# Kernel optimization log

Measured on AMD Instinct MI355X. Metric: run time of the kernel, lower is better.

Reference implementation:

```python
import jax, jax.numpy as jnp
import numpy as np

D_MODEL = 1024
NUM_HEADS = 16
HEAD_DIM = D_MODEL // NUM_HEADS
SCALE = HEAD_DIM ** -0.5
ROPE_BASE = 10000.0


def _rope_cos_sin(seq_len, dim, dtype=jnp.float32):
    inv_freq = 1.0 / (ROPE_BASE ** (jnp.arange(0, dim, 2, dtype=jnp.float32) / dim))
    t = jnp.arange(seq_len, dtype=jnp.float32)
    freqs = t[:, None] * inv_freq[None, :]            # [S, dim/2]
    emb = jnp.concatenate([freqs, freqs], axis=-1)    # [S, dim]
    # broadcast shape [1, S, 1, dim] to apply over [B, S, H, dim]
    return emb.astype(dtype)[None, :, None, :]


def _rotate_half(x):
    half = x.shape[-1] // 2
    x1, x2 = x[..., :half], x[..., half:]
    return jnp.concatenate([-x2, x1], axis=-1)


def setup_inputs() -> dict:
    key = jax.random.key(0)
    ks = jax.random.split(key, 5)
    B, S = 2, 2048
    x = jax.random.normal(ks[0], (B, S, D_MODEL), dtype=jnp.float32)
    wq = jax.random.normal(ks[1], (D_MODEL, D_MODEL), dtype=jnp.float32) * (D_MODEL ** -0.5)
    wk = jax.random.normal(ks[2], (D_MODEL, D_MODEL), dtype=jnp.float32) * (D_MODEL ** -0.5)
    wv = jax.random.normal(ks[3], (D_MODEL, D_MODEL), dtype=jnp.float32) * (D_MODEL ** -0.5)
    wo = jax.random.normal(ks[4], (D_MODEL, D_MODEL), dtype=jnp.float32) * (D_MODEL ** -0.5)
    attention_mask = jnp.tril(jnp.ones((S, S), dtype=jnp.int32))  # causal
    return {"x": x, "wq": wq, "wk": wk, "wv": wv, "wo": wo,
            "attention_mask": attention_mask}


def reference(x, wq, wk, wv, wo, attention_mask):
    B, S, _ = x.shape
    # projections (nn.Linear, no bias: y = x @ W^T)
    q = (x @ wq.T).reshape(B, S, NUM_HEADS, HEAD_DIM)
    k = (x @ wk.T).reshape(B, S, NUM_HEADS, HEAD_DIM)
    v = (x @ wv.T).reshape(B, S, NUM_HEADS, HEAD_DIM)
    # RoPE
    emb = _rope_cos_sin(S, HEAD_DIM, x.dtype)
    cos, sin = jnp.cos(emb), jnp.sin(emb)
    q = q * cos + _rotate_half(q) * sin
    k = k * cos + _rotate_half(k) * sin
    # attention scores [B, H, S, S]
    scores = jnp.einsum('bihd,bjhd->bhij', q, k) * SCALE
    mask = attention_mask[None, None, :, :]  # 2D mask -> broadcast over batch, heads
    scores = jnp.where(mask == 0, -jnp.inf, scores)
    attn = jax.nn.softmax(scores, axis=-1)
    attn = jnp.nan_to_num(attn, nan=0.0)  # fully-masked rows -> 0
    out = jnp.einsum('bhij,bjhd->bihd', attn, v).reshape(B, S, D_MODEL)
    return out @ wo.T
```

## Files before the change

kernel.cpp:

```cpp
#include <hip/hip_runtime.h>

typedef __bf16 bf16;
typedef __attribute__((ext_vector_type(8))) __bf16 bf16x8;
typedef __attribute__((ext_vector_type(4))) float f32x4;
typedef __attribute__((ext_vector_type(4))) short s16x4;
typedef __attribute__((ext_vector_type(4))) unsigned u32x4;

#define SEQ 2048
#define DM 1024
#define NH 16
#define HD 64
#define QSCALE 0.1803368801111204f

static __device__ __forceinline__ void gl_lds16(const bf16* g, bf16* l) {
  __builtin_amdgcn_global_load_lds(
      (const __attribute__((address_space(1))) void*)g,
      (__attribute__((address_space(3))) void*)l, 16, 0, 0);
}

static __device__ __forceinline__ f32x4 mfma16(bf16x8 a, bf16x8 b, f32x4 c) {
  return __builtin_amdgcn_mfma_f32_16x16x32_bf16(a, b, c, 0, 0, 0);
}

static __device__ __forceinline__ unsigned cvt_pk_bf16(float lo, float hi) {
  unsigned r;
  asm("v_cvt_pk_bf16_f32 %0, %1, %2" : "=v"(r) : "v"(lo), "v"(hi));
  return r;
}

static __device__ __forceinline__ float vmax4(f32x4 v) {
  return fmaxf(fmaxf(v[0], v[1]), fmaxf(v[2], v[3]));
}

__global__ __launch_bounds__(256)
void prep_k(const float* __restrict__ x, const float* __restrict__ wq,
            const float* __restrict__ wk, const float* __restrict__ wv,
            const float* __restrict__ wo, bf16* __restrict__ xb,
            bf16* __restrict__ wb, float* __restrict__ tab) {
  int i = blockIdx.x * 256 + threadIdx.x;
  if (i < 2097152) {
    const float* src;
    bf16* dst;
    int j;
    if (i < 1048576) {
      src = x; dst = xb; j = i;
    } else {
      j = i - 1048576;
      int seg = j >> 18;
      src = (seg == 0) ? wq : (seg == 1) ? wk : (seg == 2) ? wv : wo;
      dst = wb;
      src -= (size_t)seg << 20;
    }
    f32x4 v = ((const f32x4*)src)[j];
    s16x4 o;
#pragma unroll
    for (int q = 0; q < 4; ++q) o[q] = __builtin_bit_cast(short, (bf16)v[q]);
    ((s16x4*)dst)[j] = o;
  } else {
    int idx = i - 2097152;
    int s = idx >> 5, j = idx & 31;
    float inv = powf(10000.0f, -(float)j * (1.0f / 32.0f));
    float f = (float)s * inv;
    tab[idx * 2] = cosf(f);
    tab[idx * 2 + 1] = sinf(f);
  }
}

__global__ __launch_bounds__(256)
void gemm_qkv(const bf16* __restrict__ A, const bf16* __restrict__ B,
              bf16* __restrict__ qh, bf16* __restrict__ kh, bf16* __restrict__ vt,
              const float2* __restrict__ tab) {
  const int K = 1024;
  __shared__ __attribute__((aligned(16))) bf16 As[128 * 32];
  __shared__ __attribute__((aligned(16))) bf16 Bs[128 * 32];
  const int t = threadIdx.x;
  const int wv = t >> 6, ln = t & 63, lr = ln & 15, lg = ln >> 4;
  const int wr = wv >> 1, wc = wv & 1;
  const int l_hw = blockIdx.x + 24 * blockIdx.y;
  const int lid = (l_hw & 7) * 96 + (l_hw >> 3);
  const int m0 = (lid / 24) * 128, n0 = (lid % 24) * 128;
  const int srow = t >> 2, sslot = t & 3;
  const int seg = n0 >> 10;
  const int hh = ((n0 & 1023) + wc * 64) >> 6;

  f32x4 acc[4][4] = {};

  for (int kt = 0; kt < K; kt += 32) {
#pragma unroll
    for (int c = 0; c < 2; ++c) {
      int row = srow + (c << 6);
      int lsl = sslot ^ (row & 3);
      gl_lds16(A + (size_t)(m0 + row) * K + kt + lsl * 8, As + c * 2048 + wv * 512);
      gl_lds16(B + (size_t)(n0 + row) * K + kt + lsl * 8, Bs + c * 2048 + wv * 512);
    }
    __syncthreads();
    bf16x8 af[4], bfr[4];
#pragma unroll
    for (int i = 0; i < 4; ++i) {
      int ra = wr * 64 + i * 16 + lr;
      af[i] = *(const bf16x8*)(As + ra * 32 + ((lg ^ (ra & 3)) << 3));
      int rb = wc * 64 + i * 16 + lr;
      bfr[i] = *(const bf16x8*)(Bs + rb * 32 + ((lg ^ (rb & 3)) << 3));
    }
#pragma unroll
    for (int i = 0; i < 4; ++i)
#pragma unroll
      for (int j = 0; j < 4; ++j)
        acc[i][j] = mfma16(af[i], bfr[j], acc[i][j]);
    __syncthreads();
  }

#pragma unroll
  for (int i = 0; i < 4; ++i) {
    int row0 = m0 + wr * 64 + i * 16 + lg * 4;
    int bb = row0 >> 11, s0r = row0 & (SEQ - 1);
    if (seg < 2) {
      bf16* dst = (seg == 0) ? qh : kh;
      float scl = (seg == 0) ? QSCALE : 1.0f;
      size_t base = ((size_t)(bb * NH + hh) * SEQ + s0r) * HD;
#pragma unroll
      for (int j = 0; j < 2; ++j) {
        int dlo = j * 16 + lr;
#pragma unroll
        for (int r = 0; r < 4; ++r) {
          float2 cs = tab[(size_t)(s0r + r) * 32 + dlo];
          float a = acc[i][j][r], b2 = acc[i][j + 2][r];
          float na = (a * cs.x - b2 * cs.y) * scl;
          float nb = (b2 * cs.x + a * cs.y) * scl;
          dst[base + (size_t)r * HD + dlo] = (bf16)na;
          dst[base + (size_t)r * HD + dlo + 32] = (bf16)nb;
        }
      }
    } else {
#pragma unroll
      for (int j = 0; j < 4; ++j) {
        int d = j * 16 + lr;
        s16x4 pk;
#pragma unroll
        for (int r = 0; r < 4; ++r) pk[r] = __builtin_bit_cast(short, (bf16)acc[i][j][r]);
        *(s16x4*)(vt + ((size_t)(bb * NH + hh) * HD + d) * SEQ + s0r) = pk;
      }
    }
  }
}

__global__ __launch_bounds__(256)
void gemm_bt_f32(const bf16* __restrict__ A, const bf16* __restrict__ B,
                 float* __restrict__ C, int M, int N, int K) {
  __shared__ __attribute__((aligned(16))) bf16 As[128 * 32];
  __shared__ __attribute__((aligned(16))) bf16 Bs[128 * 32];
  const int t = threadIdx.x;
  const int wv = t >> 6, ln = t & 63, lr = ln & 15, lg = ln >> 4;
  const int wr = wv >> 1, wc = wv & 1;
  const int l_hw = blockIdx.x + 8 * blockIdx.y;
  const int lid = (l_hw & 7) * 32 + (l_hw >> 3);
  const int m0 = (lid >> 3) * 128, n0 = (lid & 7) * 128;
  const int srow = t >> 2, sslot = t & 3;

  f32x4 acc[4][4] = {};

  for (int kt = 0; kt < K; kt += 32) {
#pragma unroll
    for (int c = 0; c < 2; ++c) {
      int row = srow + (c << 6);
      int lsl = sslot ^ (row & 3);
      gl_lds16(A + (size_t)(m0 + row) * K + kt + lsl * 8, As + c * 2048 + wv * 512);
      gl_lds16(B + (size_t)(n0 + row) * K + kt + lsl * 8, Bs + c * 2048 + wv * 512);
    }
    __syncthreads();
    bf16x8 af[4], bfr[4];
#pragma unroll
    for (int i = 0; i < 4; ++i) {
      int ra = wr * 64 + i * 16 + lr;
      af[i] = *(const bf16x8*)(As + ra * 32 + ((lg ^ (ra & 3)) << 3));
      int rb = wc * 64 + i * 16 + lr;
      bfr[i] = *(const bf16x8*)(Bs + rb * 32 + ((lg ^ (rb & 3)) << 3));
    }
#pragma unroll
    for (int i = 0; i < 4; ++i)
#pragma unroll
      for (int j = 0; j < 4; ++j)
        acc[i][j] = mfma16(af[i], bfr[j], acc[i][j]);
    __syncthreads();
  }

#pragma unroll
  for (int i = 0; i < 4; ++i) {
    int row0 = m0 + wr * 64 + i * 16 + lg * 4;
#pragma unroll
    for (int j = 0; j < 4; ++j) {
      int col = n0 + wc * 64 + j * 16 + lr;
#pragma unroll
      for (int r = 0; r < 4; ++r)
        C[(size_t)(row0 + r) * N + col] = acc[i][j][r];
    }
  }
}

template <bool MASKED>
static __device__ __forceinline__ void attn_tile_lds(
    const bf16* Ksb, const bf16* Vsb, unsigned* plw,
    const bf16x8* qf, f32x4* acc, float& m_run, float& l_run,
    int lr, int lg, int qrow, int s0) {
  f32x4 sc[4] = {};
#pragma unroll
  for (int fi = 0; fi < 4; ++fi) {
    int row = fi * 16 + lr;
    int sw = row & 7;
    bf16x8 k0 = *(const bf16x8*)(Ksb + row * 64 + ((lg ^ sw) << 3));
    bf16x8 k1 = *(const bf16x8*)(Ksb + row * 64 + (((4 + lg) ^ sw) << 3));
    sc[fi] = mfma16(k0, qf[0], sc[fi]);
    sc[fi] = mfma16(k1, qf[1], sc[fi]);
  }
  if (MASKED) {
#pragma unroll
    for (int fi = 0; fi < 4; ++fi)
#pragma unroll
      for (int r = 0; r < 4; ++r) {
        int kv = s0 + fi * 16 + lg * 4 + r;
        sc[fi][r] = (kv <= qrow) ? sc[fi][r] : -3e38f;
      }
  }
  float mx = fmaxf(fmaxf(vmax4(sc[0]), vmax4(sc[1])),
                   fmaxf(vmax4(sc[2]), vmax4(sc[3])));
  mx = fmaxf(mx, __shfl_xor(mx, 16));
  mx = fmaxf(mx, __shfl_xor(mx, 32));
  if (!__all(mx <= m_run)) {
    float mn = fmaxf(m_run, mx);
    float alpha = __builtin_amdgcn_exp2f(m_run - mn);
    m_run = mn;
    l_run *= alpha;
#pragma unroll
    for (int d0 = 0; d0 < 4; ++d0)
#pragma unroll
      for (int r = 0; r < 4; ++r) acc[d0][r] *= alpha;
  }
  float pf[4][4], sm = 0.0f;
#pragma unroll
  for (int fi = 0; fi < 4; ++fi)
#pragma unroll
    for (int r = 0; r < 4; ++r) {
      pf[fi][r] = __builtin_amdgcn_exp2f(sc[fi][r] - m_run);
      sm += pf[fi][r];
    }
  sm += __shfl_xor(sm, 16);
  sm += __shfl_xor(sm, 32);
  l_run += sm;

  const int sw2 = (lr & 7) << 2;
#pragma unroll
  for (int fi = 0; fi < 4; ++fi)
#pragma unroll
    for (int hh = 0; hh < 2; ++hh)
      plw[lr * 32 + ((fi * 8 + lg * 2 + hh) ^ sw2)] =
          cvt_pk_bf16(pf[fi][2 * hh], pf[fi][2 * hh + 1]);
  asm volatile("s_waitcnt lgkmcnt(0)" ::: "memory");
  __builtin_amdgcn_sched_barrier(0);
#pragma unroll
  for (int kc = 0; kc < 2; ++kc) {
    u32x4 praw = *(const u32x4*)(plw + lr * 32 + ((kc * 16 + lg * 4) ^ sw2));
    bf16x8 pb = __builtin_bit_cast(bf16x8, praw);
#pragma unroll
    for (int d0 = 0; d0 < 4; ++d0) {
      int row = d0 * 16 + lr;
      int sw = row & 7;
      bf16x8 vf = *(const bf16x8*)(Vsb + row * 64 + (((kc * 4 + lg) ^ sw) << 3));
      acc[d0] = mfma16(vf, pb, acc[d0]);
    }
  }
  asm volatile("" ::: "memory");
}

__global__ __launch_bounds__(256, 4)
void attn_k(const bf16* __restrict__ qh, const bf16* __restrict__ kh,
            const bf16* __restrict__ vt, bf16* __restrict__ ao) {
  __shared__ __attribute__((aligned(16))) bf16 Ks[2][64 * 64];
  __shared__ __attribute__((aligned(16))) bf16 Vs[2][64 * 64];
  __shared__ __attribute__((aligned(16))) unsigned plds[4][512];

  const int t = threadIdx.x, wv = t >> 6, ln = t & 63, lr = ln & 15, lg = ln >> 4;
  const int bid = blockIdx.x;
  const int xcd = bid & 7, g = bid >> 3;
  const int bh = xcd * 4 + (g & 3);
  const int qt = 31 - (g >> 2);
  const int b = bh >> 4, h = bh & 15;

  const bf16* qp = qh + (size_t)bh * SEQ * HD;
  const bf16* kp = kh + (size_t)bh * SEQ * HD;
  const bf16* vp = vt + (size_t)bh * HD * SEQ;
  unsigned* plw = &plds[wv][0];

  const int qrow = qt * 64 + wv * 16 + lr;

  bf16x8 qf[2];
  qf[0] = *(const bf16x8*)(qp + (size_t)qrow * HD + lg * 8);
  qf[1] = *(const bf16x8*)(qp + (size_t)qrow * HD + 32 + lg * 8);

  f32x4 acc[4] = {};
  float m_run = -3e38f, l_run = 0.0f;

  const int nt = qt + 1;

  auto STAGE = [&](int buf, int tt) {
    int s0 = tt * 64;
#pragma unroll
    for (int c = 0; c < 2; ++c) {
      int rA = wv * 16 + c * 8;
      int row = rA + (ln >> 3);
      int sl = (ln & 7) ^ (row & 7);
      gl_lds16(kp + (size_t)(s0 + row) * HD + (sl << 3), &Ks[buf][rA * 64]);
      gl_lds16(vp + (size_t)row * SEQ + s0 + (sl << 3), &Vs[buf][rA * 64]);
    }
  };

  STAGE(0, 0);
  asm volatile("s_waitcnt vmcnt(0)" ::: "memory");
  __builtin_amdgcn_s_barrier();

  int cur = 0;
  for (int tt = 0; tt < nt; ++tt) {
    if (tt + 1 < nt) STAGE(cur ^ 1, tt + 1);
    if (tt == qt)
      attn_tile_lds<true>(&Ks[cur][0], &Vs[cur][0], plw, qf, acc, m_run, l_run,
                          lr, lg, qrow, tt * 64);
    else
      attn_tile_lds<false>(&Ks[cur][0], &Vs[cur][0], plw, qf, acc, m_run, l_run,
                           lr, lg, qrow, tt * 64);
    asm volatile("s_waitcnt vmcnt(0)" ::: "memory");
    __builtin_amdgcn_s_barrier();
    cur ^= 1;
  }

  float invl = 1.0f / l_run;
  bf16* aop = ao + ((size_t)b * SEQ + qrow) * DM + h * HD;
#pragma unroll
  for (int d0 = 0; d0 < 4; ++d0) {
    unsigned lo = cvt_pk_bf16(acc[d0][0] * invl, acc[d0][1] * invl);
    unsigned hi = cvt_pk_bf16(acc[d0][2] * invl, acc[d0][3] * invl);
    uint2 pk; pk.x = lo; pk.y = hi;
    *(uint2*)(aop + d0 * 16 + lg * 4) = pk;
  }
}

extern "C" void kernel_launch(void* const* d_in, const int* in_sizes, int n_in,
                              void* d_out, int out_size, void* d_ws, size_t ws_size,
                              hipStream_t stream) {
  const float* x = (const float*)d_in[0];
  const float* wq = (const float*)d_in[1];
  const float* wk = (const float*)d_in[2];
  const float* wv = (const float*)d_in[3];
  const float* wo = (const float*)d_in[4];

  char* ws = (char*)d_ws;
  const size_t MB = 1ull << 20;
  bf16* xb    = (bf16*)ws;
  bf16* wqkvb = (bf16*)(ws + 8 * MB);
  bf16* wob   = (bf16*)(ws + 14 * MB);
  bf16* qhb   = (bf16*)(ws + 16 * MB);
  bf16* khb   = (bf16*)(ws + 24 * MB);
  bf16* vtb   = (bf16*)(ws + 32 * MB);
  float* tab  = (float*)(ws + 40 * MB);
  bf16* aob = xb;

  prep_k<<<8448, 256, 0, stream>>>(x, wq, wk, wv, wo, xb, wqkvb, tab);

  gemm_qkv<<<dim3(24, 32), 256, 0, stream>>>(xb, wqkvb, qhb, khb, vtb, (const float2*)tab);

  attn_k<<<1024, 256, 0, stream>>>(qhb, khb, vtb, aob);

  gemm_bt_f32<<<dim3(8, 32), 256, 0, stream>>>(aob, wob, (float*)d_out, 4096, 1024, 1024);
}
```

Measured before the change: 118.8 us.

## Double-buffer LDS tiles in QKV and output projection GEMMs

Both projection GEMMs now use two LDS buffers per operand and issue the global-to-LDS loads for the next K-tile before computing on the current one. A single vmcnt wait and barrier per iteration replaces the two syncthreads. This is meant to overlap global memory latency with MFMA work. It doubles LDS use per block, which may lower occupancy.

```diff
diff --git a/kernel.cpp b/kernel.cpp
--- a/kernel.cpp
+++ b/kernel.cpp
@@ -71,8 +71,8 @@
               bf16* __restrict__ qh, bf16* __restrict__ kh, bf16* __restrict__ vt,
               const float2* __restrict__ tab) {
   const int K = 1024;
-  __shared__ __attribute__((aligned(16))) bf16 As[128 * 32];
-  __shared__ __attribute__((aligned(16))) bf16 Bs[128 * 32];
+  __shared__ __attribute__((aligned(16))) bf16 As[2][128 * 32];
+  __shared__ __attribute__((aligned(16))) bf16 Bs[2][128 * 32];
   const int t = threadIdx.x;
   const int wv = t >> 6, ln = t & 63, lr = ln & 15, lg = ln >> 4;
   const int wr = wv >> 1, wc = wv & 1;
@@ -85,29 +85,39 @@
 
   f32x4 acc[4][4] = {};
 
-  for (int kt = 0; kt < K; kt += 32) {
+  auto STAGE = [&](int buf, int kt) {
 #pragma unroll
     for (int c = 0; c < 2; ++c) {
       int row = srow + (c << 6);
       int lsl = sslot ^ (row & 3);
-      gl_lds16(A + (size_t)(m0 + row) * K + kt + lsl * 8, As + c * 2048 + wv * 512);
-      gl_lds16(B + (size_t)(n0 + row) * K + kt + lsl * 8, Bs + c * 2048 + wv * 512);
-    }
-    __syncthreads();
+      gl_lds16(A + (size_t)(m0 + row) * K + kt + lsl * 8, &As[buf][0] + c * 2048 + wv * 512);
+      gl_lds16(B + (size_t)(n0 + row) * K + kt + lsl * 8, &Bs[buf][0] + c * 2048 + wv * 512);
+    }
+  };
+
+  STAGE(0, 0);
+  asm volatile("s_waitcnt vmcnt(0)" ::: "memory");
+  __builtin_amdgcn_s_barrier();
+
+  int cur = 0;
+  for (int kt = 0; kt < K; kt += 32) {
+    if (kt + 32 < K) STAGE(cur ^ 1, kt + 32);
     bf16x8 af[4], bfr[4];
 #pragma unroll
     for (int i = 0; i < 4; ++i) {
       int ra = wr * 64 + i * 16 + lr;
-      af[i] = *(const bf16x8*)(As + ra * 32 + ((lg ^ (ra & 3)) << 3));
+      af[i] = *(const bf16x8*)(&As[cur][0] + ra * 32 + ((lg ^ (ra & 3)) << 3));
       int rb = wc * 64 + i * 16 + lr;
-      bfr[i] = *(const bf16x8*)(Bs + rb * 32 + ((lg ^ (rb & 3)) << 3));
+      bfr[i] = *(const bf16x8*)(&Bs[cur][0] + rb * 32 + ((lg ^ (rb & 3)) << 3));
     }
 #pragma unroll
     for (int i = 0; i < 4; ++i)
 #pragma unroll
       for (int j = 0; j < 4; ++j)
         acc[i][j] = mfma16(af[i], bfr[j], acc[i][j]);
-    __syncthreads();
+    asm volatile("s_waitcnt vmcnt(0)" ::: "memory");
+    __builtin_amdgcn_s_barrier();
+    cur ^= 1;
   }
 
 #pragma unroll
@@ -147,8 +157,8 @@
 __global__ __launch_bounds__(256)
 void gemm_bt_f32(const bf16* __restrict__ A, const bf16* __restrict__ B,
                  float* __restrict__ C, int M, int N, int K) {
-  __shared__ __attribute__((aligned(16))) bf16 As[128 * 32];
-  __shared__ __attribute__((aligned(16))) bf16 Bs[128 * 32];
+  __shared__ __attribute__((aligned(16))) bf16 As[2][128 * 32];
+  __shared__ __attribute__((aligned(16))) bf16 Bs[2][128 * 32];
   const int t = threadIdx.x;
   const int wv = t >> 6, ln = t & 63, lr = ln & 15, lg = ln >> 4;
   const int wr = wv >> 1, wc = wv & 1;
@@ -159,29 +169,39 @@
 
   f32x4 acc[4][4] = {};
 
-  for (int kt = 0; kt < K; kt += 32) {
+  auto STAGE = [&](int buf, int kt) {
 #pragma unroll
     for (int c = 0; c < 2; ++c) {
       int row = srow + (c << 6);
       int lsl = sslot ^ (row & 3);
-      gl_lds16(A + (size_t)(m0 + row) * K + kt + lsl * 8, As + c * 2048 + wv * 512);
-      gl_lds16(B + (size_t)(n0 + row) * K + kt + lsl * 8, Bs + c * 2048 + wv * 512);
-    }
-    __syncthreads();
+      gl_lds16(A + (size_t)(m0 + row) * K + kt + lsl * 8, &As[buf][0] + c * 2048 + wv * 512);
+      gl_lds16(B + (size_t)(n0 + row) * K + kt + lsl * 8, &Bs[buf][0] + c * 2048 + wv * 512);
+    }
+  };
+
+  STAGE(0, 0);
+  asm volatile("s_waitcnt vmcnt(0)" ::: "memory");
+  __builtin_amdgcn_s_barrier();
+
+  int cur = 0;
+  for (int kt = 0; kt < K; kt += 32) {
+    if (kt + 32 < K) STAGE(cur ^ 1, kt + 32);
     bf16x8 af[4], bfr[4];
 #pragma unroll
     for (int i = 0; i < 4; ++i) {
       int ra = wr * 64 + i * 16 + lr;
-      af[i] = *(const bf16x8*)(As + ra * 32 + ((lg ^ (ra & 3)) << 3));
+      af[i] = *(const bf16x8*)(&As[cur][0] + ra * 32 + ((lg ^ (ra & 3)) << 3));
       int rb = wc * 64 + i * 16 + lr;
-      bfr[i] = *(const bf16x8*)(Bs + rb * 32 + ((lg ^ (rb & 3)) << 3));
+      bfr[i] = *(const bf16x8*)(&Bs[cur][0] + rb * 32 + ((lg ^ (rb & 3)) << 3));
     }
 #pragma unroll
     for (int i = 0; i < 4; ++i)
 #pragma unroll
       for (int j = 0; j < 4; ++j)
         acc[i][j] = mfma16(af[i], bfr[j], acc[i][j]);
-    __syncthreads();
+    asm volatile("s_waitcnt vmcnt(0)" ::: "memory");
+    __builtin_amdgcn_s_barrier();
+    cur ^= 1;
   }
 
 #pragma unroll
```

Measured after the change: 131.6 us. +10.7%, slower.
